# Optimization experiments

Hardware: AMD Instinct MI355X
Metric: run time of the kernel (lower is better)

Reference implementation:

```python
import jax, jax.numpy as jnp
import numpy as np

OUT, IN = 5632, 2048
GROUP_SIZE = 128
N_GROUPS = (OUT * IN) // GROUP_SIZE
LORA_SCALE = 32.0 / 16.0  # lora_alpha / lora_r


def dequantize_int4(packed, scales, zeros):
    # packed: [numel//2], each byte holds two 4-bit codes (low nibble first)
    low = packed & 0xF
    high = (packed >> 4) & 0xF
    q = jnp.stack([low, high], axis=-1).reshape(-1).astype(jnp.float32)  # [numel]
    q = q.reshape(N_GROUPS, GROUP_SIZE)
    w = (q - zeros[:, None]) * scales[:, None]
    return w.reshape(OUT, IN)


def setup_inputs() -> dict:
    key = jax.random.key(0)
    k1, k2, k3, k4, k5, k6 = jax.random.split(key, 6)
    x = jax.random.normal(k1, (4, 2048, IN), dtype=jnp.float32)
    packed = jax.random.randint(k2, ((OUT * IN) // 2,), 0, 256, dtype=jnp.int32)
    scales = jax.random.uniform(k3, (N_GROUPS,), dtype=jnp.float32) * 0.02 + 1e-3
    zeros = jax.random.uniform(k4, (N_GROUPS,), dtype=jnp.float32) * 15.0
    lora_A = jax.random.normal(k5, (IN, 16), dtype=jnp.float32) * (1.0 / np.sqrt(IN))
    lora_B = jax.random.normal(k6, (16, OUT), dtype=jnp.float32) * 0.02
    return {"x": x, "packed": packed, "scales": scales, "zeros": zeros,
            "lora_A": lora_A, "lora_B": lora_B}


def reference(x, packed, scales, zeros, lora_A, lora_B):
    W = dequantize_int4(packed, scales, zeros)            # [OUT, IN]
    base = jnp.einsum('bsi,oi->bso', x, W)                # F.linear(x, W)
    lora = ((x @ lora_A) @ lora_B) * LORA_SCALE           # low-rank path
    return base + lora
```

## Files before the change

kernel.cpp:

```cpp
#include <hip/hip_runtime.h>

#define M_DIM 8192
#define K_DIM 2048
#define N_DIM 5632

typedef __attribute__((ext_vector_type(8))) short short8;
typedef __attribute__((ext_vector_type(4))) float f32x4;

__device__ __forceinline__ short f2b(float f) {
  union { float f; unsigned u; } v; v.f = f;
  unsigned r = v.u + 0x7FFFu + ((v.u >> 16) & 1u);
  return (short)(r >> 16);
}

__device__ __forceinline__ void async16(void* lds, const void* g) {
  __builtin_amdgcn_global_load_lds(
      (const __attribute__((address_space(1))) unsigned*)g,
      (__attribute__((address_space(3))) unsigned*)lds,
      16, 0, 0);
}

__global__ __launch_bounds__(256) void cvt_x_kernel(const float* __restrict__ x,
                                                    short* __restrict__ xb) {
  long t = (long)blockIdx.x * 256 + threadIdx.x;
  const float4* xv = (const float4*)x;
  float4 f0 = xv[2 * t];
  float4 f1 = xv[2 * t + 1];
  short8 o;
  o[0] = f2b(f0.x); o[1] = f2b(f0.y); o[2] = f2b(f0.z); o[3] = f2b(f0.w);
  o[4] = f2b(f1.x); o[5] = f2b(f1.y); o[6] = f2b(f1.z); o[7] = f2b(f1.w);
  *(short8*)(xb + 8 * t) = o;
}

__global__ __launch_bounds__(256) void dequant_lora_kernel(
    const int* __restrict__ packed, const float* __restrict__ scales,
    const float* __restrict__ zeros, const float* __restrict__ lA,
    const float* __restrict__ lB, short* __restrict__ wb) {
  int o = blockIdx.x;
  int i0 = threadIdx.x * 8;
  long e0 = (long)o * K_DIM + i0;
  int4 p = ((const int4*)packed)[e0 >> 3];
  int g = (int)(e0 >> 7);
  float s = scales[g], z = zeros[g];

  float bcol[16];
#pragma unroll
  for (int r = 0; r < 16; ++r) bcol[r] = lB[r * N_DIM + o] * 2.0f;

  short8 out8;
#pragma unroll
  for (int d = 0; d < 4; ++d) {
    int pv = (&p.x)[d];
    float w0 = ((float)(pv & 0xF) - z) * s;
    float w1 = ((float)((pv >> 4) & 0xF) - z) * s;
    const float4* a0 = (const float4*)&lA[(i0 + 2 * d) * 16];
    const float4* a1 = (const float4*)&lA[(i0 + 2 * d + 1) * 16];
    float acc0 = 0.f, acc1 = 0.f;
#pragma unroll
    for (int r4 = 0; r4 < 4; ++r4) {
      float4 av0 = a0[r4], av1 = a1[r4];
      acc0 += av0.x * bcol[4 * r4] + av0.y * bcol[4 * r4 + 1] +
              av0.z * bcol[4 * r4 + 2] + av0.w * bcol[4 * r4 + 3];
      acc1 += av1.x * bcol[4 * r4] + av1.y * bcol[4 * r4 + 1] +
              av1.z * bcol[4 * r4 + 2] + av1.w * bcol[4 * r4 + 3];
    }
    out8[2 * d] = f2b(w0 + acc0);
    out8[2 * d + 1] = f2b(w1 + acc1);
  }
  *(short8*)(wb + e0) = out8;
}

__global__ __launch_bounds__(512, 2) void gemm_kernel(const short* __restrict__ xb,
                                                      const short* __restrict__ wb,
                                                      float* __restrict__ out) {
  __shared__ __align__(16) short lds[65536];

  const int tid = threadIdx.x;
  const int lane = tid & 63;
  const int wave = tid >> 6;
  const int wm = wave >> 2, wn = wave & 3;
  const int l15 = lane & 15, quad = lane >> 4;

  int flat = blockIdx.x;
  int swz = (flat & 7) * 88 + (flat >> 3);
  int bm = swz / 22, bn = swz - bm * 22;
  const int m0 = bm * 256, n0 = bn * 256;

  const short* a_base = xb + (size_t)m0 * K_DIM;
  const short* b_base = wb + (size_t)n0 * K_DIM;

  const int rswz = quad ^ ((l15 >> 1) & 3);
  const int a_rd = (wm * 128 + l15) * 32 + rswz * 8;
  const int b_rd = 32768 + (wn * 64 + l15) * 32 + rswz * 8;

  const int srow = tid >> 2;
  const int schunk = (tid & 3) ^ ((srow >> 1) & 3);
  const short* ag0 = a_base + (size_t)srow * K_DIM + schunk * 8;
  const short* ag1 = ag0 + (size_t)128 * K_DIM;
  const short* bg0 = b_base + (size_t)srow * K_DIM + schunk * 8;
  const short* bg1 = bg0 + (size_t)128 * K_DIM;
  const int sl0 = tid * 8, sl1 = (512 + tid) * 8;

  f32x4 acc[8][4] = {};

#pragma unroll
  for (int t = 0; t < 3; ++t) {
    const int sb = t * 8192;
    async16(&lds[sb + sl0], ag0 + t * 32);
    async16(&lds[sb + sl1], ag1 + t * 32);
    async16(&lds[32768 + sb + sl0], bg0 + t * 32);
    async16(&lds[32768 + sb + sl1], bg1 + t * 32);
  }
  asm volatile("s_waitcnt vmcnt(8)" ::: "memory");
  __builtin_amdgcn_s_barrier();

  auto tile = [&](int k, bool do_stage) {
    const int bo = (k & 3) * 8192;
    const int so = ((k + 3) & 3) * 8192;
    short8 bf[4], af[4];
#pragma unroll
    for (int ni = 0; ni < 4; ++ni)
      bf[ni] = *(const short8*)&lds[bo + b_rd + ni * 512];
#pragma unroll
    for (int mi = 0; mi < 4; ++mi)
      af[mi] = *(const short8*)&lds[bo + a_rd + mi * 512];
    if (do_stage) {
      async16(&lds[so + sl0], ag0 + (k + 3) * 32);
      async16(&lds[so + sl1], ag1 + (k + 3) * 32);
    }
    __builtin_amdgcn_s_barrier();
    __builtin_amdgcn_s_setprio(1);
#pragma unroll
    for (int mi = 0; mi < 4; ++mi)
#pragma unroll
      for (int ni = 0; ni < 4; ++ni)
        acc[mi][ni] = __builtin_amdgcn_mfma_f32_16x16x32_bf16(
            af[mi], bf[ni], acc[mi][ni], 0, 0, 0);
    __builtin_amdgcn_s_setprio(0);
    __builtin_amdgcn_s_barrier();
#pragma unroll
    for (int mi = 0; mi < 4; ++mi)
      af[mi] = *(const short8*)&lds[bo + a_rd + (4 + mi) * 512];
    if (do_stage) {
      async16(&lds[32768 + so + sl0], bg0 + (k + 3) * 32);
      async16(&lds[32768 + so + sl1], bg1 + (k + 3) * 32);
    }
    __builtin_amdgcn_s_barrier();
    __builtin_amdgcn_s_setprio(1);
#pragma unroll
    for (int mi = 0; mi < 4; ++mi)
#pragma unroll
      for (int ni = 0; ni < 4; ++ni)
        acc[4 + mi][ni] = __builtin_amdgcn_mfma_f32_16x16x32_bf16(
            af[mi], bf[ni], acc[4 + mi][ni], 0, 0, 0);
    __builtin_amdgcn_s_setprio(0);
  };

#pragma unroll 1
  for (int k = 0; k < 61; ++k) {
    tile(k, true);
    asm volatile("s_waitcnt vmcnt(8)" ::: "memory");
    __builtin_amdgcn_s_barrier();
  }
  tile(61, false);
  asm volatile("s_waitcnt vmcnt(4)" ::: "memory");
  __builtin_amdgcn_s_barrier();
  tile(62, false);
  asm volatile("s_waitcnt vmcnt(0)" ::: "memory");
  __builtin_amdgcn_s_barrier();
  tile(63, false);

  float* op = out + (size_t)(m0 + wm * 128 + quad * 4) * N_DIM + n0 + wn * 64 + l15;
#pragma unroll
  for (int mi = 0; mi < 8; ++mi)
#pragma unroll
    for (int r = 0; r < 4; ++r)
#pragma unroll
      for (int ni = 0; ni < 4; ++ni)
        op[(size_t)(mi * 16 + r) * N_DIM + ni * 16] = acc[mi][ni][r];
}

extern "C" void kernel_launch(void* const* d_in, const int* in_sizes, int n_in,
                              void* d_out, int out_size, void* d_ws, size_t ws_size,
                              hipStream_t stream) {
  const float* x      = (const float*)d_in[0];
  const int*   packed = (const int*)d_in[1];
  const float* scales = (const float*)d_in[2];
  const float* zeros  = (const float*)d_in[3];
  const float* lA     = (const float*)d_in[4];
  const float* lB     = (const float*)d_in[5];
  float* out = (float*)d_out;

  short* xb = (short*)d_ws;
  short* wb = xb + (size_t)M_DIM * K_DIM;

  cvt_x_kernel<<<(M_DIM * K_DIM) / (256 * 8), 256, 0, stream>>>(x, xb);
  dequant_lora_kernel<<<N_DIM, 256, 0, stream>>>(packed, scales, zeros, lA, lB, wb);
  gemm_kernel<<<dim3(N_DIM / 256 * (M_DIM / 256)), 512, 0, stream>>>(xb, wb, out);
}
```

Before: 519.2 us.

## Double-buffer LDS fragments in GEMM, transpose LoRA A, narrow x conversion

The GEMM main loop now prefetches the next tile's A and B register fragments while running the current tile's MFMAs. It drops the two intra-tile barriers and issues all four async global-to-LDS stages together. A new kernel transposes and pre-scales lora_A into scratch space at the end of the output buffer, so the dequant kernel reads contiguous rows of A. The x conversion kernel now handles four elements per thread instead of eight. The register-level double buffering raises VGPR pressure, and the reduced barriers with altered waitcnt values risk LDS race hazards.

After: 456.9 us. -12.0%, faster.

```diff
diff --git a/kernel.cpp b/kernel.cpp
--- a/kernel.cpp
+++ b/kernel.cpp
@@ -5,6 +5,7 @@
 #define N_DIM 5632
 
 typedef __attribute__((ext_vector_type(8))) short short8;
+typedef __attribute__((ext_vector_type(4))) short s4v;
 typedef __attribute__((ext_vector_type(4))) float f32x4;
 
 __device__ __forceinline__ short f2b(float f) {
@@ -23,18 +24,26 @@
 __global__ __launch_bounds__(256) void cvt_x_kernel(const float* __restrict__ x,
                                                     short* __restrict__ xb) {
   long t = (long)blockIdx.x * 256 + threadIdx.x;
-  const float4* xv = (const float4*)x;
-  float4 f0 = xv[2 * t];
-  float4 f1 = xv[2 * t + 1];
-  short8 o;
-  o[0] = f2b(f0.x); o[1] = f2b(f0.y); o[2] = f2b(f0.z); o[3] = f2b(f0.w);
-  o[4] = f2b(f1.x); o[5] = f2b(f1.y); o[6] = f2b(f1.z); o[7] = f2b(f1.w);
-  *(short8*)(xb + 8 * t) = o;
+  float4 f = ((const float4*)x)[t];
+  s4v o;
+  o[0] = f2b(f.x); o[1] = f2b(f.y); o[2] = f2b(f.z); o[3] = f2b(f.w);
+  *(s4v*)(xb + 4 * t) = o;
+}
+
+__global__ __launch_bounds__(256) void lat_kernel(const float* __restrict__ lA,
+                                                  float* __restrict__ lAT) {
+  int i = blockIdx.x * 256 + threadIdx.x;
+  const float4* row = (const float4*)(lA + (size_t)i * 16);
+  float4 v0 = row[0], v1 = row[1], v2 = row[2], v3 = row[3];
+  float vals[16] = {v0.x, v0.y, v0.z, v0.w, v1.x, v1.y, v1.z, v1.w,
+                    v2.x, v2.y, v2.z, v2.w, v3.x, v3.y, v3.z, v3.w};
+#pragma unroll
+  for (int r = 0; r < 16; ++r) lAT[r * K_DIM + i] = vals[r] * 2.0f;
 }
 
 __global__ __launch_bounds__(256) void dequant_lora_kernel(
     const int* __restrict__ packed, const float* __restrict__ scales,
-    const float* __restrict__ zeros, const float* __restrict__ lA,
+    const float* __restrict__ zeros, const float* __restrict__ lAT,
     const float* __restrict__ lB, short* __restrict__ wb) {
   int o = blockIdx.x;
   int i0 = threadIdx.x * 8;
@@ -43,30 +52,26 @@
   int g = (int)(e0 >> 7);
   float s = scales[g], z = zeros[g];
 
-  float bcol[16];
-#pragma unroll
-  for (int r = 0; r < 16; ++r) bcol[r] = lB[r * N_DIM + o] * 2.0f;
-
-  short8 out8;
+  float accv[8];
 #pragma unroll
   for (int d = 0; d < 4; ++d) {
     int pv = (&p.x)[d];
-    float w0 = ((float)(pv & 0xF) - z) * s;
-    float w1 = ((float)((pv >> 4) & 0xF) - z) * s;
-    const float4* a0 = (const float4*)&lA[(i0 + 2 * d) * 16];
-    const float4* a1 = (const float4*)&lA[(i0 + 2 * d + 1) * 16];
-    float acc0 = 0.f, acc1 = 0.f;
-#pragma unroll
-    for (int r4 = 0; r4 < 4; ++r4) {
-      float4 av0 = a0[r4], av1 = a1[r4];
-      acc0 += av0.x * bcol[4 * r4] + av0.y * bcol[4 * r4 + 1] +
-              av0.z * bcol[4 * r4 + 2] + av0.w * bcol[4 * r4 + 3];
-      acc1 += av1.x * bcol[4 * r4] + av1.y * bcol[4 * r4 + 1] +
-              av1.z * bcol[4 * r4 + 2] + av1.w * bcol[4 * r4 + 3];
-    }
-    out8[2 * d] = f2b(w0 + acc0);
-    out8[2 * d + 1] = f2b(w1 + acc1);
-  }
+    accv[2 * d]     = ((float)(pv & 0xF) - z) * s;
+    accv[2 * d + 1] = ((float)((pv >> 4) & 0xF) - z) * s;
+  }
+#pragma unroll
+  for (int r = 0; r < 16; ++r) {
+    float b = lB[r * N_DIM + o];
+    const float4* ar = (const float4*)&lAT[r * K_DIM + i0];
+    float4 a0 = ar[0], a1 = ar[1];
+    accv[0] += a0.x * b; accv[1] += a0.y * b;
+    accv[2] += a0.z * b; accv[3] += a0.w * b;
+    accv[4] += a1.x * b; accv[5] += a1.y * b;
+    accv[6] += a1.z * b; accv[7] += a1.w * b;
+  }
+  short8 out8;
+#pragma unroll
+  for (int j = 0; j < 8; ++j) out8[j] = f2b(accv[j]);
   *(short8*)(wb + e0) = out8;
 }
 
@@ -102,6 +107,7 @@
   const int sl0 = tid * 8, sl1 = (512 + tid) * 8;
 
   f32x4 acc[8][4] = {};
+  short8 bfA[4], af1A[4], bfB[4], af1B[4];
 
 #pragma unroll
   for (int t = 0; t < 3; ++t) {
@@ -111,64 +117,69 @@
     async16(&lds[32768 + sb + sl0], bg0 + t * 32);
     async16(&lds[32768 + sb + sl1], bg1 + t * 32);
   }
-  asm volatile("s_waitcnt vmcnt(8)" ::: "memory");
+  asm volatile("s_waitcnt vmcnt(4)" ::: "memory");
   __builtin_amdgcn_s_barrier();
-
-  auto tile = [&](int k, bool do_stage) {
+#pragma unroll
+  for (int ni = 0; ni < 4; ++ni) bfA[ni] = *(const short8*)&lds[b_rd + ni * 512];
+#pragma unroll
+  for (int mi = 0; mi < 4; ++mi) af1A[mi] = *(const short8*)&lds[a_rd + mi * 512];
+
+  auto tile = [&](int k, short8* bfc, short8* af1c, short8* bfn, short8* af1n,
+                  bool do_stage, bool do_pref) {
     const int bo = (k & 3) * 8192;
+    const int no_ = ((k + 1) & 3) * 8192;
     const int so = ((k + 3) & 3) * 8192;
-    short8 bf[4], af[4];
-#pragma unroll
-    for (int ni = 0; ni < 4; ++ni)
-      bf[ni] = *(const short8*)&lds[bo + b_rd + ni * 512];
+    short8 af2[4];
 #pragma unroll
     for (int mi = 0; mi < 4; ++mi)
-      af[mi] = *(const short8*)&lds[bo + a_rd + mi * 512];
+      af2[mi] = *(const short8*)&lds[bo + a_rd + (4 + mi) * 512];
+    if (do_pref) {
+#pragma unroll
+      for (int ni = 0; ni < 4; ++ni)
+        bfn[ni] = *(const short8*)&lds[no_ + b_rd + ni * 512];
+#pragma unroll
+      for (int mi = 0; mi < 4; ++mi)
+        af1n[mi] = *(const short8*)&lds[no_ + a_rd + mi * 512];
+    }
     if (do_stage) {
       async16(&lds[so + sl0], ag0 + (k + 3) * 32);
       async16(&lds[so + sl1], ag1 + (k + 3) * 32);
-    }
-    __builtin_amdgcn_s_barrier();
-    __builtin_amdgcn_s_setprio(1);
-#pragma unroll
-    for (int mi = 0; mi < 4; ++mi)
-#pragma unroll
-      for (int ni = 0; ni < 4; ++ni)
-        acc[mi][ni] = __builtin_amdgcn_mfma_f32_16x16x32_bf16(
-            af[mi], bf[ni], acc[mi][ni], 0, 0, 0);
-    __builtin_amdgcn_s_setprio(0);
-    __builtin_amdgcn_s_barrier();
-#pragma unroll
-    for (int mi = 0; mi < 4; ++mi)
-      af[mi] = *(const short8*)&lds[bo + a_rd + (4 + mi) * 512];
-    if (do_stage) {
       async16(&lds[32768 + so + sl0], bg0 + (k + 3) * 32);
       async16(&lds[32768 + so + sl1], bg1 + (k + 3) * 32);
     }
-    __builtin_amdgcn_s_barrier();
     __builtin_amdgcn_s_setprio(1);
 #pragma unroll
     for (int mi = 0; mi < 4; ++mi)
 #pragma unroll
       for (int ni = 0; ni < 4; ++ni)
+        acc[mi][ni] = __builtin_amdgcn_mfma_f32_16x16x32_bf16(
+            af1c[mi], bfc[ni], acc[mi][ni], 0, 0, 0);
+#pragma unroll
+    for (int mi = 0; mi < 4; ++mi)
+#pragma unroll
+      for (int ni = 0; ni < 4; ++ni)
         acc[4 + mi][ni] = __builtin_amdgcn_mfma_f32_16x16x32_bf16(
-            af[mi], bf[ni], acc[4 + mi][ni], 0, 0, 0);
+            af2[mi], bfc[ni], acc[4 + mi][ni], 0, 0, 0);
     __builtin_amdgcn_s_setprio(0);
   };
 
 #pragma unroll 1
-  for (int k = 0; k < 61; ++k) {
-    tile(k, true);
-    asm volatile("s_waitcnt vmcnt(8)" ::: "memory");
+  for (int k = 0; k < 60; k += 2) {
+    tile(k, bfA, af1A, bfB, af1B, true, true);
+    asm volatile("s_waitcnt vmcnt(4)" ::: "memory");
     __builtin_amdgcn_s_barrier();
-  }
-  tile(61, false);
+    tile(k + 1, bfB, af1B, bfA, af1A, true, true);
+    asm volatile("s_waitcnt vmcnt(4)" ::: "memory");
+    __builtin_amdgcn_s_barrier();
+  }
+  tile(60, bfA, af1A, bfB, af1B, true, true);
   asm volatile("s_waitcnt vmcnt(4)" ::: "memory");
   __builtin_amdgcn_s_barrier();
-  tile(62, false);
+  tile(61, bfB, af1B, bfA, af1A, false, true);
   asm volatile("s_waitcnt vmcnt(0)" ::: "memory");
   __builtin_amdgcn_s_barrier();
-  tile(63, false);
+  tile(62, bfA, af1A, bfB, af1B, false, true);
+  tile(63, bfB, af1B, bfA, af1A, false, false);
 
   float* op = out + (size_t)(m0 + wm * 128 + quad * 4) * N_DIM + n0 + wn * 64 + l15;
 #pragma unroll
@@ -193,8 +204,10 @@
 
   short* xb = (short*)d_ws;
   short* wb = xb + (size_t)M_DIM * K_DIM;
-
-  cvt_x_kernel<<<(M_DIM * K_DIM) / (256 * 8), 256, 0, stream>>>(x, xb);
-  dequant_lora_kernel<<<N_DIM, 256, 0, stream>>>(packed, scales, zeros, lA, lB, wb);
+  float* lAT = out + ((size_t)4 * 2048 * N_DIM - 16 * K_DIM);
+
+  cvt_x_kernel<<<(M_DIM * K_DIM) / (256 * 4), 256, 0, stream>>>(x, xb);
+  lat_kernel<<<K_DIM / 256, 256, 0, stream>>>(lA, lAT);
+  dequant_lora_kernel<<<N_DIM, 256, 0, stream>>>(packed, scales, zeros, lAT, lB, wb);
   gemm_kernel<<<dim3(N_DIM / 256 * (M_DIM / 256)), 512, 0, stream>>>(xb, wb, out);
 }
```
